# Kernel tuning notes

Measured on AMD Instinct MI355X. Metric: run time of the kernel, lower is better.

Reference implementation:

```python
import jax, jax.numpy as jnp
import numpy as np
from jax.scipy.linalg import solve_triangular

B, T, HID = 1, 2048, 2048
HK, DK = 16, 96
HV, DV = 16, 192
KDIM, VDIM = HK * DK, HV * DV
KCONV = 4
CHUNK = 64
EPS = 1e-6


def setup_inputs():
    key = jax.random.key(0)
    ks = jax.random.split(key, 16)
    s = 0.02
    return {
        "hidden_states": jax.random.normal(ks[0], (B, T, HID), jnp.float32),
        "Wq": jax.random.normal(ks[1], (HID, KDIM), jnp.float32) * s,
        "Wk": jax.random.normal(ks[2], (HID, KDIM), jnp.float32) * s,
        "Wv": jax.random.normal(ks[3], (HID, VDIM), jnp.float32) * s,
        "Wb": jax.random.normal(ks[4], (HID, HV), jnp.float32) * s,
        "Wa": jax.random.normal(ks[5], (HID, HV), jnp.float32) * s,
        "Wg": jax.random.normal(ks[6], (HID, VDIM), jnp.float32) * s,
        "Wo": jax.random.normal(ks[7], (VDIM, HID), jnp.float32) * s,
        "conv_q": jax.random.normal(ks[8], (KDIM, KCONV), jnp.float32) * 0.5,
        "conv_k": jax.random.normal(ks[9], (KDIM, KCONV), jnp.float32) * 0.5,
        "conv_v": jax.random.normal(ks[10], (VDIM, KCONV), jnp.float32) * 0.5,
        "A_log": jnp.log(jax.random.uniform(ks[11], (HV,), jnp.float32, 1.0, 16.0)),
        "dt_bias": jax.random.uniform(ks[12], (HV,), jnp.float32, 0.0, 1.0),
        "norm_weight": jnp.ones((DV,), jnp.float32),
    }


def short_conv_silu(x, w):
    # x: [B,T,C], w: [C,K]; causal depthwise conv (left pad K-1) then SiLU
    K = w.shape[-1]
    xp = jnp.pad(x, ((0, 0), (K - 1, 0), (0, 0)))
    y = sum(xp[:, j:j + x.shape[1], :] * w[:, j] for j in range(K))
    return jax.nn.silu(y)


def l2norm(x):
    return x * jax.lax.rsqrt(jnp.sum(x * x, axis=-1, keepdims=True) + EPS)


def chunk_gated_delta_rule(q, k, v, g, beta):
    # q,k: [B,T,H,dk]; v: [B,T,H,dv]; g,beta: [B,T,H]. Chunked parallel scan (WY form).
    Bb, Tt, H, dk = q.shape
    dv = v.shape[-1]
    N = Tt // CHUNK
    q = l2norm(q) * (dk ** -0.5)
    k = l2norm(k)
    chunk = lambda x: x.transpose(0, 2, 1, 3).reshape(Bb, H, N, CHUNK, x.shape[-1])
    qc, kc, vc = chunk(q), chunk(k), chunk(v)
    gc = jnp.cumsum(g.transpose(0, 2, 1).reshape(Bb, H, N, CHUNK), axis=-1)
    bc = beta.transpose(0, 2, 1).reshape(Bb, H, N, CHUNK)

    m_inc = jnp.tril(jnp.ones((CHUNK, CHUNK), bool))
    m_str = jnp.tril(jnp.ones((CHUNK, CHUNK), bool), -1)
    diff = gc[..., :, None] - gc[..., None, :]
    D = jnp.exp(jnp.where(m_inc, diff, 0.0)) * m_inc  # [B,H,N,C,C] intra-chunk decay

    kb = kc * bc[..., None]
    A = -jnp.einsum('bhnik,bhnjk->bhnij', kb, kc) * D * m_str
    eye = jnp.eye(CHUNK, dtype=q.dtype)
    # UT transform: Tm = (I - A)^{-1}, A strictly lower triangular
    Tm = solve_triangular(eye - A, jnp.broadcast_to(eye, A.shape), lower=True, unit_diagonal=True)
    u = Tm @ (vc * bc[..., None])                   # [B,H,N,C,dv]
    w = Tm @ (kb * jnp.exp(gc)[..., None])          # [B,H,N,C,dk]
    g_last = gc[..., -1]                            # [B,H,N]

    def step(S, inp):
        q_i, k_i, u_i, w_i, g_i, D_i, gl = inp
        v_new = u_i - w_i @ S                       # [B,H,C,dv]
        attn = jnp.einsum('bhik,bhjk->bhij', q_i, k_i) * D_i
        o_i = (q_i * jnp.exp(g_i)[..., None]) @ S + attn @ v_new
        k_dec = k_i * jnp.exp(gl[..., None] - g_i)[..., None]
        S = S * jnp.exp(gl)[..., None, None] + jnp.einsum('bhck,bhcv->bhkv', k_dec, v_new)
        return S, o_i

    mv = lambda x: jnp.moveaxis(x, 2, 0)
    S0 = jnp.zeros((Bb, H, dk, dv), q.dtype)
    _, o = jax.lax.scan(step, S0, (mv(qc), mv(kc), mv(u), mv(w), mv(gc), mv(D), mv(g_last)))
    o = jnp.moveaxis(o, 0, 2).reshape(Bb, H, Tt, dv)
    return o.transpose(0, 2, 1, 3)                  # [B,T,H,dv]


def reference(hidden_states, Wq, Wk, Wv, Wb, Wa, Wg, Wo, conv_q, conv_k, conv_v, A_log, dt_bias, norm_weight):
    q = short_conv_silu(hidden_states @ Wq, conv_q).reshape(B, T, HK, DK)
    k = short_conv_silu(hidden_states @ Wk, conv_k).reshape(B, T, HK, DK)
    v = short_conv_silu(hidden_states @ Wv, conv_v).reshape(B, T, HV, DV)
    beta = jax.nn.sigmoid(hidden_states @ Wb) * 2.0          # allow_neg_eigval -> beta in [0,2]
    g = -jnp.exp(A_log) * jax.nn.softplus(hidden_states @ Wa + dt_bias)  # log decay, [B,T,HV]
    o = chunk_gated_delta_rule(q, k, v, g, beta)             # [B,T,HV,DV]
    gate = (hidden_states @ Wg).reshape(B, T, HV, DV)
    o = o * jax.nn.silu(gate)                                # gated RMSNorm (gate, then norm)
    o = o * jax.lax.rsqrt(jnp.mean(o * o, axis=-1, keepdims=True) + EPS) * norm_weight
    return o.reshape(B, T, VDIM) @ Wo
```

## Files before the change

### kernel.cpp

```cpp
#include <hip/hip_runtime.h>
#include <math.h>

#define T_LEN 2048
#define HIDN  2048
#define HKN   16
#define DKN   96
#define HVN   16
#define DVN   192
#define KDIMN 1536
#define VDIMN 3072
#define QKVD  6144
#define CHUNKN 64
#define NCHUNK 32
#define EPSF 1e-6f
#define TN_STRIDE 10240

typedef __attribute__((ext_vector_type(8))) short short8;
typedef __attribute__((ext_vector_type(4))) float f32x4;

__device__ __forceinline__ unsigned short f2bf(float f) {
    unsigned int u = __float_as_uint(f);
    unsigned int r = (u + 0x7FFFu + ((u >> 16) & 1u)) >> 16;
    return (unsigned short)r;
}
__device__ __forceinline__ float bf2f(unsigned short u) {
    return __uint_as_float(((unsigned int)u) << 16);
}
__device__ __forceinline__ float siluf(float x) { return x / (1.f + expf(-x)); }

__device__ __forceinline__ void gld_lds16(const void* g, void* l) {
    __builtin_amdgcn_global_load_lds((const __attribute__((address_space(1))) unsigned int*)g,
                                     (__attribute__((address_space(3))) unsigned int*)l, 16, 0, 0);
}

__global__ void cast_f32_bf16(const float* __restrict__ in, unsigned short* __restrict__ out, int n) {
    int i = (blockIdx.x * blockDim.x + threadIdx.x) * 4;
    if (i >= n) return;
    float4 v = *(const float4*)(in + i);
    ushort4 o;
    o.x = f2bf(v.x); o.y = f2bf(v.y); o.z = f2bf(v.z); o.w = f2bf(v.w);
    *(ushort4*)(out + i) = o;
}

__global__ void transpose_cast(const float* __restrict__ W, unsigned short* __restrict__ Wt,
                               int K, int N) {
    __shared__ float tile[64][65];
    int k0 = blockIdx.y * 64, n0 = blockIdx.x * 64;
    int tx = threadIdx.x, ty = threadIdx.y;
    for (int r = ty; r < 64; r += 4) tile[r][tx] = W[(size_t)(k0 + r) * N + n0 + tx];
    __syncthreads();
    for (int r = ty; r < 64; r += 4) Wt[(size_t)(n0 + r) * K + k0 + tx] = f2bf(tile[tx][r]);
}

__global__ __launch_bounds__(256) void gemm_bt2(const unsigned short* __restrict__ A,
                                                const unsigned short* __restrict__ Bt,
                                                float* __restrict__ C1, int ld1, int nblk1,
                                                unsigned short* __restrict__ C2, int ld2,
                                                int M, int K) {
    __shared__ __align__(16) unsigned short As[2][128 * 32];
    __shared__ __align__(16) unsigned short Bs[2][128 * 32];
    int tid = threadIdx.x;
    int wave = tid >> 6, lane = tid & 63;
    int bm = blockIdx.y, bn = blockIdx.x;
    f32x4 acc[4][4] = {};
    int wr = wave >> 1, wc = wave & 1;
    int rstage = wave * 32 + (lane >> 2);
    int cstage = (lane & 3) * 8;
    const size_t a_row0 = (size_t)bm * 128;
    const size_t b_row0 = (size_t)bn * 128;
    const unsigned short* gaBase = A + (a_row0 + rstage) * (size_t)K + cstage;
    const unsigned short* gbBase = Bt + (b_row0 + rstage) * (size_t)K + cstage;
    int row_a[4], row_b[4];
#pragma unroll
    for (int i = 0; i < 4; ++i) {
        row_a[i] = wr * 64 + i * 16 + (lane & 15);
        row_b[i] = wc * 64 + i * 16 + (lane & 15);
    }
    int koff = (lane >> 4) * 8;
    int niter = K >> 5;
    {
        unsigned short* ab = &As[0][wave * 1024];
        unsigned short* bb = &Bs[0][wave * 1024];
        gld_lds16(gaBase, ab);
        gld_lds16(gaBase + (size_t)16 * K, ab + 512);
        gld_lds16(gbBase, bb);
        gld_lds16(gbBase + (size_t)16 * K, bb + 512);
    }
    __syncthreads();
    for (int i = 0; i < niter; ++i) {
        int cur = i & 1;
        if (i + 1 < niter) {
            int k0 = (i + 1) * 32;
            unsigned short* ab = &As[cur ^ 1][wave * 1024];
            unsigned short* bb = &Bs[cur ^ 1][wave * 1024];
            gld_lds16(gaBase + k0, ab);
            gld_lds16(gaBase + k0 + (size_t)16 * K, ab + 512);
            gld_lds16(gbBase + k0, bb);
            gld_lds16(gbBase + k0 + (size_t)16 * K, bb + 512);
        }
        short8 af[4], bfr[4];
#pragma unroll
        for (int mi = 0; mi < 4; ++mi) af[mi] = *(const short8*)&As[cur][row_a[mi] * 32 + koff];
#pragma unroll
        for (int ni = 0; ni < 4; ++ni) bfr[ni] = *(const short8*)&Bs[cur][row_b[ni] * 32 + koff];
#pragma unroll
        for (int mi = 0; mi < 4; ++mi)
#pragma unroll
            for (int ni = 0; ni < 4; ++ni)
                acc[mi][ni] = __builtin_amdgcn_mfma_f32_16x16x32_bf16(af[mi], bfr[ni], acc[mi][ni], 0, 0, 0);
        __syncthreads();
    }
    if (bn < nblk1) {
        int colb = bn * 128;
#pragma unroll
        for (int mi = 0; mi < 4; ++mi) {
            int rbase = bm * 128 + wr * 64 + mi * 16 + (lane >> 4) * 4;
#pragma unroll
            for (int ni = 0; ni < 4; ++ni) {
                int col = colb + wc * 64 + ni * 16 + (lane & 15);
#pragma unroll
                for (int j = 0; j < 4; ++j)
                    C1[(size_t)(rbase + j) * ld1 + col] = acc[mi][ni][j];
            }
        }
    } else {
        int colb = (bn - nblk1) * 128;
#pragma unroll
        for (int mi = 0; mi < 4; ++mi) {
            int rbase = bm * 128 + wr * 64 + mi * 16 + (lane >> 4) * 4;
#pragma unroll
            for (int ni = 0; ni < 4; ++ni) {
                int col = colb + wc * 64 + ni * 16 + (lane & 15);
#pragma unroll
                for (int j = 0; j < 4; ++j)
                    C2[(size_t)(rbase + j) * ld2 + col] = f2bf(acc[mi][ni][j]);
            }
        }
    }
}

__global__ __launch_bounds__(256) void gemm_btk(const unsigned short* __restrict__ A,
                                                const unsigned short* __restrict__ Bt,
                                                float* __restrict__ C, float* __restrict__ Cp,
                                                int M, int N, int K) {
    __shared__ __align__(16) unsigned short As[2][128 * 32];
    __shared__ __align__(16) unsigned short Bs[2][128 * 32];
    int tid = threadIdx.x;
    int wave = tid >> 6, lane = tid & 63;
    int bm = blockIdx.y, bn = blockIdx.x, kz = blockIdx.z;
    int kchunk = K / 3;
    int kbeg = kz * kchunk;
    f32x4 acc[4][4] = {};
    int wr = wave >> 1, wc = wave & 1;
    int rstage = wave * 32 + (lane >> 2);
    int cstage = (lane & 3) * 8;
    const size_t a_row0 = (size_t)bm * 128;
    const size_t b_row0 = (size_t)bn * 128;
    const unsigned short* gaBase = A + (a_row0 + rstage) * (size_t)K + kbeg + cstage;
    const unsigned short* gbBase = Bt + (b_row0 + rstage) * (size_t)K + kbeg + cstage;
    int row_a[4], row_b[4];
#pragma unroll
    for (int i = 0; i < 4; ++i) {
        row_a[i] = wr * 64 + i * 16 + (lane & 15);
        row_b[i] = wc * 64 + i * 16 + (lane & 15);
    }
    int koff = (lane >> 4) * 8;
    int niter = kchunk >> 5;
    {
        unsigned short* ab = &As[0][wave * 1024];
        unsigned short* bb = &Bs[0][wave * 1024];
        gld_lds16(gaBase, ab);
        gld_lds16(gaBase + (size_t)16 * K, ab + 512);
        gld_lds16(gbBase, bb);
        gld_lds16(gbBase + (size_t)16 * K, bb + 512);
    }
    __syncthreads();
    for (int i = 0; i < niter; ++i) {
        int cur = i & 1;
        if (i + 1 < niter) {
            int k0 = (i + 1) * 32;
            unsigned short* ab = &As[cur ^ 1][wave * 1024];
            unsigned short* bb = &Bs[cur ^ 1][wave * 1024];
            gld_lds16(gaBase + k0, ab);
            gld_lds16(gaBase + k0 + (size_t)16 * K, ab + 512);
            gld_lds16(gbBase + k0, bb);
            gld_lds16(gbBase + k0 + (size_t)16 * K, bb + 512);
        }
        short8 af[4], bfr[4];
#pragma unroll
        for (int mi = 0; mi < 4; ++mi) af[mi] = *(const short8*)&As[cur][row_a[mi] * 32 + koff];
#pragma unroll
        for (int ni = 0; ni < 4; ++ni) bfr[ni] = *(const short8*)&Bs[cur][row_b[ni] * 32 + koff];
#pragma unroll
        for (int mi = 0; mi < 4; ++mi)
#pragma unroll
            for (int ni = 0; ni < 4; ++ni)
                acc[mi][ni] = __builtin_amdgcn_mfma_f32_16x16x32_bf16(af[mi], bfr[ni], acc[mi][ni], 0, 0, 0);
        __syncthreads();
    }
    float* Cout = (kz == 0) ? C : (Cp + (size_t)(kz - 1) * M * N);
#pragma unroll
    for (int mi = 0; mi < 4; ++mi) {
        int rbase = bm * 128 + wr * 64 + mi * 16 + (lane >> 4) * 4;
#pragma unroll
        for (int ni = 0; ni < 4; ++ni) {
            int col = bn * 128 + wc * 64 + ni * 16 + (lane & 15);
#pragma unroll
            for (int j = 0; j < 4; ++j)
                Cout[(size_t)(rbase + j) * N + col] = acc[mi][ni][j];
        }
    }
}

__global__ void addk(float* __restrict__ out, const float* __restrict__ p, int n) {
    int i = (blockIdx.x * blockDim.x + threadIdx.x) * 4;
    if (i >= n) return;
    float4 a = *(const float4*)(out + i);
    float4 b = *(const float4*)(p + i);
    float4 c = *(const float4*)(p + n + i);
    a.x += b.x + c.x; a.y += b.y + c.y; a.z += b.z + c.z; a.w += b.w + c.w;
    *(float4*)(out + i) = a;
}

__global__ void conv_silu_all(const float* __restrict__ pre,
                              const float* __restrict__ cq, const float* __restrict__ ck,
                              const float* __restrict__ cv, float* __restrict__ out) {
    int c = blockIdx.x * blockDim.x + threadIdx.x;
    int t = blockIdx.y;
    const float* wc4 = (c < 1536) ? (cq + (size_t)c * 4)
                     : (c < 3072) ? (ck + (size_t)(c - 1536) * 4)
                                  : (cv + (size_t)(c - 3072) * 4);
    float acc = 0.f;
    if (t >= 3) acc += pre[(size_t)(t - 3) * QKVD + c] * wc4[0];
    if (t >= 2) acc += pre[(size_t)(t - 2) * QKVD + c] * wc4[1];
    if (t >= 1) acc += pre[(size_t)(t - 1) * QKVD + c] * wc4[2];
    acc += pre[(size_t)t * QKVD + c] * wc4[3];
    out[(size_t)t * QKVD + c] = siluf(acc);
}

__global__ __launch_bounds__(256) void beta_g(const float* __restrict__ X,
                                              const float* __restrict__ Wb, const float* __restrict__ Wa,
                                              const float* __restrict__ A_log, const float* __restrict__ dtb,
                                              float* __restrict__ bvec, float* __restrict__ gvec) {
    int t = blockIdx.x;
    int tid = threadIdx.x;
    int cg = tid & 7, ks = tid >> 3;
    int wave = tid >> 6, lane = tid & 63;
    const float* xr = X + (size_t)t * HIDN;
    const float* Wsel = (cg < 4) ? Wb : Wa;
    int cc = (cg & 3) * 4;
    float ax = 0.f, ay = 0.f, az = 0.f, aw = 0.f;
#pragma unroll 4
    for (int i = 0; i < 16; ++i) {
        int k = (ks + 32 * i) * 4;
        float4 xv = *(const float4*)(xr + k);
        float4 w0 = *(const float4*)(Wsel + (size_t)(k + 0) * 16 + cc);
        float4 w1 = *(const float4*)(Wsel + (size_t)(k + 1) * 16 + cc);
        float4 w2 = *(const float4*)(Wsel + (size_t)(k + 2) * 16 + cc);
        float4 w3 = *(const float4*)(Wsel + (size_t)(k + 3) * 16 + cc);
        ax += xv.x * w0.x + xv.y * w1.x + xv.z * w2.x + xv.w * w3.x;
        ay += xv.x * w0.y + xv.y * w1.y + xv.z * w2.y + xv.w * w3.y;
        az += xv.x * w0.z + xv.y * w1.z + xv.z * w2.z + xv.w * w3.z;
        aw += xv.x * w0.w + xv.y * w1.w + xv.z * w2.w + xv.w * w3.w;
    }
#pragma unroll
    for (int off = 8; off <= 32; off <<= 1) {
        ax += __shfl_xor(ax, off, 64);
        ay += __shfl_xor(ay, off, 64);
        az += __shfl_xor(az, off, 64);
        aw += __shfl_xor(aw, off, 64);
    }
    __shared__ float red[4][8][4];
    if ((lane >> 3) == 0) {
        red[wave][cg][0] = ax; red[wave][cg][1] = ay;
        red[wave][cg][2] = az; red[wave][cg][3] = aw;
    }
    __syncthreads();
    if (tid < 8) {
        float tot[4];
#pragma unroll
        for (int j = 0; j < 4; ++j)
            tot[j] = red[0][tid][j] + red[1][tid][j] + red[2][tid][j] + red[3][tid][j];
        int c0 = (tid & 3) * 4;
        if (tid < 4) {
#pragma unroll
            for (int j = 0; j < 4; ++j)
                bvec[(size_t)t * 16 + c0 + j] = 2.f / (1.f + expf(-tot[j]));
        } else {
#pragma unroll
            for (int j = 0; j < 4; ++j) {
                float a = tot[j] + dtb[c0 + j];
                float sp = (a > 20.f) ? a : log1pf(expf(a));
                gvec[(size_t)t * 16 + c0 + j] = -expf(A_log[c0 + j]) * sp;
            }
        }
    }
}

__global__ __launch_bounds__(256) void phase1_mfma(
    const float* __restrict__ qkv, const float* __restrict__ gvec,
    const float* __restrict__ bvec,
    float* __restrict__ u_ws, float* __restrict__ w_ws,
    float* __restrict__ qg_ws, float* __restrict__ at_ws,
    float* __restrict__ gl_ws, float* __restrict__ Ct,
    unsigned short* __restrict__ Tn) {
    int n = blockIdx.x, h = blockIdx.y;
    int t0 = n * CHUNKN;
    int tid = threadIdx.x;
    int wave = tid >> 6, lane = tid & 63;
    size_t base = (size_t)(h * NCHUNK + n);

    __shared__ __align__(16) char LB1[139776];
    unsigned short* QKb  = (unsigned short*)(LB1 + 0);
    unsigned short* Pb   = (unsigned short*)(LB1 + 26624);
    unsigned short* RHSw = (unsigned short*)(LB1 + 39936);
    unsigned short* RHSv = (unsigned short*)(LB1 + 53760);
    unsigned short* Ab   = (unsigned short*)(LB1 + 81408);
    unsigned short* Atb  = (unsigned short*)(LB1 + 94720);
    unsigned short* Ptb  = (unsigned short*)(LB1 + 108032);
    float*          Pf   = (float*)(LB1 + 121344);
    unsigned short* kdT  = (unsigned short*)(LB1 + 81408);
    unsigned short* wT   = (unsigned short*)(LB1 + 95232);
    unsigned short* uT   = (unsigned short*)(LB1 + 109056);
    float* gr_s = (float*)(LB1 + 138752);
    float* gc_s = gr_s + 64;
    float* be_s = gc_s + 64;
    float* egc  = be_s + 64;

    if (tid < 64) {
        gr_s[tid] = gvec[(size_t)(t0 + tid) * HVN + h];
        be_s[tid] = bvec[(size_t)(t0 + tid) * HVN + h];
    }
    __syncthreads();
    if (tid < 64) {
        float sacc = 0.f;
        for (int j = 0; j <= tid; ++j) sacc += gr_s[j];
        gc_s[tid] = sacc;
    }
    __syncthreads();
    float gl = gc_s[63];
    if (tid < 64) egc[tid] = expf(gl - gc_s[tid]);

    int r = tid >> 2, sub = tid & 3;
    {
        const float* kp = qkv + (size_t)(t0 + r) * QKVD + 1536 + h * DKN + sub * 24;
        float kreg[24];
        float ss = 0.f;
#pragma unroll
        for (int i = 0; i < 6; ++i) {
            float4 v = *(const float4*)(kp + i * 4);
            kreg[i * 4 + 0] = v.x; kreg[i * 4 + 1] = v.y; kreg[i * 4 + 2] = v.z; kreg[i * 4 + 3] = v.w;
            ss += v.x * v.x + v.y * v.y + v.z * v.z + v.w * v.w;
        }
        ss += __shfl_xor(ss, 1, 64);
        ss += __shfl_xor(ss, 2, 64);
        float nrm = rsqrtf(ss + EPSF);
        float gcr = gc_s[r];
        float ebg = be_s[r] * expf(gcr);
#pragma unroll
        for (int i = 0; i < 24; ++i) {
            float kn = kreg[i] * nrm;
            QKb[r * 104 + sub * 24 + i] = f2bf(kn);
            RHSw[(sub * 24 + i) * 72 + r] = f2bf(kn * ebg);
        }
    }
    {
        const float* qp = qkv + (size_t)(t0 + r) * QKVD + 0 + h * DKN + sub * 24;
        float qreg[24];
        float ss = 0.f;
#pragma unroll
        for (int i = 0; i < 6; ++i) {
            float4 v = *(const float4*)(qp + i * 4);
            qreg[i * 4 + 0] = v.x; qreg[i * 4 + 1] = v.y; qreg[i * 4 + 2] = v.z; qreg[i * 4 + 3] = v.w;
            ss += v.x * v.x + v.y * v.y + v.z * v.z + v.w * v.w;
        }
        ss += __shfl_xor(ss, 1, 64);
        ss += __shfl_xor(ss, 2, 64);
        float nrm = rsqrtf(ss + EPSF) * 0.10206207261596577f;
        float eg = expf(gc_s[r]);
        float* qgp = qg_ws + base * (64 * 96) + r * 96 + sub * 24;
#pragma unroll
        for (int i = 0; i < 24; ++i) {
            float qn = qreg[i] * nrm;
            QKb[(64 + r) * 104 + sub * 24 + i] = f2bf(qn);
            qgp[i] = qn * eg;
        }
    }
    {
        const float* vp = qkv + (size_t)(t0 + r) * QKVD + 3072 + h * DVN + sub * 48;
        float ber = be_s[r];
#pragma unroll
        for (int i = 0; i < 12; ++i) {
            float4 v = *(const float4*)(vp + i * 4);
            int d = sub * 48 + i * 4;
            RHSv[(d + 0) * 72 + r] = f2bf(v.x * ber);
            RHSv[(d + 1) * 72 + r] = f2bf(v.y * ber);
            RHSv[(d + 2) * 72 + r] = f2bf(v.z * ber);
            RHSv[(d + 3) * 72 + r] = f2bf(v.w * ber);
        }
    }
    __syncthreads();

    {
        f32x4 acc1[2][4] = {};
#pragma unroll
        for (int ks = 0; ks < 3; ++ks) {
            int ko = ks * 32 + (lane >> 4) * 8;
            short8 af[2], bfv[4];
#pragma unroll
            for (int rt2 = 0; rt2 < 2; ++rt2)
                af[rt2] = *(const short8*)&QKb[(wave * 32 + rt2 * 16 + (lane & 15)) * 104 + ko];
#pragma unroll
            for (int ct = 0; ct < 4; ++ct)
                bfv[ct] = *(const short8*)&QKb[(ct * 16 + (lane & 15)) * 104 + ko];
#pragma unroll
            for (int rt2 = 0; rt2 < 2; ++rt2)
#pragma unroll
                for (int ct = 0; ct < 4; ++ct)
                    acc1[rt2][ct] = __builtin_amdgcn_mfma_f32_16x16x32_bf16(af[rt2], bfv[ct], acc1[rt2][ct], 0, 0, 0);
        }
#pragma unroll
        for (int rt2 = 0; rt2 < 2; ++rt2)
#pragma unroll
            for (int ct = 0; ct < 4; ++ct)
#pragma unroll
                for (int j = 0; j < 4; ++j) {
                    int rr = wave * 32 + rt2 * 16 + (lane >> 4) * 4 + j;
                    int cc = ct * 16 + (lane & 15);
                    float val = acc1[rt2][ct][j];
                    if (rr < 64) {
                        float av = (rr > cc) ? -be_s[rr] * expf(gc_s[rr] - gc_s[cc]) * val : 0.f;
                        unsigned short ab = f2bf(av);
                        Ab[rr * 104 + cc] = ab;
                        Atb[cc * 104 + rr] = ab;
                        float pv = (rr == cc) ? 1.f : av;
                        Pf[rr * 68 + cc] = pv;
                        unsigned short pb = f2bf(pv);
                        Pb[rr * 104 + cc] = pb;
                        Ptb[cc * 104 + rr] = pb;
                    } else {
                        int ar = rr - 64;
                        float av = (ar >= cc) ? expf(gc_s[ar] - gc_s[cc]) * val : 0.f;
                        at_ws[base * (64 * 64) + ar * 64 + cc] = av;
                    }
                }
    }
    __syncthreads();

#pragma unroll 1
    for (int lev = 0; lev < 5; ++lev) {
        f32x4 d[4] = {};
#pragma unroll
        for (int ks = 0; ks < 2; ++ks) {
            int ko = ks * 32 + (lane >> 4) * 8;
            short8 a0 = *(const short8*)&Ab[(wave * 16 + (lane & 15)) * 104 + ko];
#pragma unroll
            for (int ct = 0; ct < 4; ++ct) {
                short8 b0 = *(const short8*)&Atb[(ct * 16 + (lane & 15)) * 104 + ko];
                d[ct] = __builtin_amdgcn_mfma_f32_16x16x32_bf16(a0, b0, d[ct], 0, 0, 0);
            }
        }
        __syncthreads();
#pragma unroll
        for (int ct = 0; ct < 4; ++ct)
#pragma unroll
            for (int j = 0; j < 4; ++j) {
                int rr = wave * 16 + (lane >> 4) * 4 + j;
                int cc = ct * 16 + (lane & 15);
                unsigned short hb = f2bf(d[ct][j]);
                Ab[rr * 104 + cc] = hb;
                Atb[cc * 104 + rr] = hb;
            }
        __syncthreads();
        f32x4 e[4];
#pragma unroll
        for (int ct = 0; ct < 4; ++ct)
#pragma unroll
            for (int j = 0; j < 4; ++j)
                e[ct][j] = Pf[(wave * 16 + (lane >> 4) * 4 + j) * 68 + ct * 16 + (lane & 15)];
#pragma unroll
        for (int ks = 0; ks < 2; ++ks) {
            int ko = ks * 32 + (lane >> 4) * 8;
            short8 a0 = *(const short8*)&Ab[(wave * 16 + (lane & 15)) * 104 + ko];
#pragma unroll
            for (int ct = 0; ct < 4; ++ct) {
                short8 b0 = *(const short8*)&Ptb[(ct * 16 + (lane & 15)) * 104 + ko];
                e[ct] = __builtin_amdgcn_mfma_f32_16x16x32_bf16(a0, b0, e[ct], 0, 0, 0);
            }
        }
        __syncthreads();
#pragma unroll
        for (int ct = 0; ct < 4; ++ct)
#pragma unroll
            for (int j = 0; j < 4; ++j) {
                int rr = wave * 16 + (lane >> 4) * 4 + j;
                int cc = ct * 16 + (lane & 15);
                float pv = e[ct][j];
                Pf[rr * 68 + cc] = pv;
                unsigned short pb = f2bf(pv);
                Pb[rr * 104 + cc] = pb;
                Ptb[cc * 104 + rr] = pb;
            }
        __syncthreads();
    }

    for (int f = tid; f < 6144; f += 256) {
        int d = f >> 6, tt = f & 63;
        kdT[d * 72 + tt] = f2bf(bf2f(QKb[tt * 104 + d]) * egc[tt]);
    }

#pragma unroll 1
    for (int i = 0; i < 18; ++i) {
        int id = wave * 18 + i;
        int rt = id & 3, ct = id >> 2;
        f32x4 o4 = {};
#pragma unroll
        for (int ks = 0; ks < 2; ++ks) {
            int ko = ks * 32 + (lane >> 4) * 8;
            short8 a0 = *(const short8*)&Pb[(rt * 16 + (lane & 15)) * 104 + ko];
            short8 b0 = (ct < 12)
                ? *(const short8*)&RHSv[(ct * 16 + (lane & 15)) * 72 + ko]
                : *(const short8*)&RHSw[((ct - 12) * 16 + (lane & 15)) * 72 + ko];
            o4 = __builtin_amdgcn_mfma_f32_16x16x32_bf16(a0, b0, o4, 0, 0, 0);
        }
#pragma unroll
        for (int j = 0; j < 4; ++j) {
            int rr = rt * 16 + (lane >> 4) * 4 + j;
            int nn = ct * 16 + (lane & 15);
            if (ct < 12) {
                u_ws[base * (64 * 192) + rr * 192 + nn] = o4[j];
                uT[nn * 72 + rr] = f2bf(o4[j]);
            } else {
                w_ws[base * (64 * 96) + rr * 96 + (nn - 192)] = o4[j];
                wT[(nn - 192) * 72 + rr] = f2bf(o4[j]);
            }
        }
    }
    __syncthreads();

    float eglv = expf(gl);
#pragma unroll 1
    for (int q = 0; q < 27; ++q) {
        int id = wave * 27 + q;
        f32x4 acc = {};
        if (id < 36) {
            int jt = id / 6, kt = id % 6;
#pragma unroll
            for (int ks = 0; ks < 2; ++ks) {
                int ko = ks * 32 + (lane >> 4) * 8;
                short8 a0 = *(const short8*)&kdT[(jt * 16 + (lane & 15)) * 72 + ko];
                short8 b0 = *(const short8*)&wT[(kt * 16 + (lane & 15)) * 72 + ko];
                acc = __builtin_amdgcn_mfma_f32_16x16x32_bf16(a0, b0, acc, 0, 0, 0);
            }
#pragma unroll
            for (int rr = 0; rr < 4; ++rr) {
                int j = jt * 16 + (lane >> 4) * 4 + rr;
                int k = kt * 16 + (lane & 15);
                float val = -acc[rr];
                if (j == k) val += eglv;
                Tn[base * TN_STRIDE + j * 104 + k] = f2bf(val);
            }
        } else {
            int cid = id - 36;
            int it = cid / 6, jt = cid % 6;
#pragma unroll
            for (int ks = 0; ks < 2; ++ks) {
                int ko = ks * 32 + (lane >> 4) * 8;
                short8 a0 = *(const short8*)&uT[(it * 16 + (lane & 15)) * 72 + ko];
                short8 b0 = *(const short8*)&kdT[(jt * 16 + (lane & 15)) * 72 + ko];
                acc = __builtin_amdgcn_mfma_f32_16x16x32_bf16(a0, b0, acc, 0, 0, 0);
            }
#pragma unroll
            for (int rr = 0; rr < 4; ++rr)
                Ct[base * 18432 + (size_t)(it * 16 + (lane >> 4) * 4 + rr) * 96 + jt * 16 + (lane & 15)] = acc[rr];
        }
    }
    if (tid == 0) gl_ws[base] = gl;
}

__global__ __launch_bounds__(128) void mscan(const float* __restrict__ Ct, const unsigned short* __restrict__ Tn,
                                             float* __restrict__ s_ws) {
    int rg = blockIdx.x, h = blockIdx.y;
    int tid = threadIdx.x, wave = tid >> 6, lane = tid & 63;
    __shared__ __align__(16) unsigned short St[48 * 104];
    __shared__ __align__(16) unsigned short TnB[2][TN_STRIDE];
    __shared__ __align__(16) float CtB[2][48 * 96];
    for (int i = tid; i < 48 * 104; i += 128) St[i] = 0;

    {
        const float* cp = Ct + (size_t)(h * NCHUNK) * 18432 + rg * (48 * 96);
        const unsigned short* tp = Tn + (size_t)(h * NCHUNK) * TN_STRIDE;
#pragma unroll
        for (int q = 0; q < 9; ++q) {
            size_t o = (size_t)(wave * 9 + q) * 1024 + lane * 16;
            gld_lds16((const char*)cp + o, (char*)&CtB[0][0] + (size_t)(wave * 9 + q) * 1024);
        }
#pragma unroll
        for (int q = 0; q < 10; ++q) {
            size_t o = (size_t)(wave * 10 + q) * 1024 + lane * 16;
            gld_lds16((const char*)tp + o, (char*)&TnB[0][0] + (size_t)(wave * 10 + q) * 1024);
        }
    }
    f32x4 acc[3][3] = {};
    int colw = wave * 48;
    __syncthreads();

#pragma unroll 1
    for (int n = 0; n < NCHUNK; ++n) {
        size_t base = (size_t)(h * NCHUNK + n);
        int cur = n & 1;
        if (n + 1 < NCHUNK) {
            const float* cp = Ct + (base + 1) * 18432 + rg * (48 * 96);
            const unsigned short* tp = Tn + (base + 1) * TN_STRIDE;
#pragma unroll
            for (int q = 0; q < 9; ++q) {
                size_t o = (size_t)(wave * 9 + q) * 1024 + lane * 16;
                gld_lds16((const char*)cp + o, (char*)&CtB[cur ^ 1][0] + (size_t)(wave * 9 + q) * 1024);
            }
#pragma unroll
            for (int q = 0; q < 10; ++q) {
                size_t o = (size_t)(wave * 10 + q) * 1024 + lane * 16;
                gld_lds16((const char*)tp + o, (char*)&TnB[cur ^ 1][0] + (size_t)(wave * 10 + q) * 1024);
            }
        }
        float* sp = s_ws + base * 18432 + rg * (48 * 96);
#pragma unroll
        for (int it = 0; it < 3; ++it)
#pragma unroll
            for (int jt = 0; jt < 3; ++jt) {
                int irow = it * 16 + (lane >> 4) * 4;
                int col = colw + jt * 16 + (lane & 15);
#pragma unroll
                for (int r = 0; r < 4; ++r) {
                    sp[(size_t)(irow + r) * 96 + col] = acc[it][jt][r];
                    acc[it][jt][r] = CtB[cur][(irow + r) * 96 + col];
                }
            }
#pragma unroll
        for (int ks = 0; ks < 3; ++ks) {
            int ko = ks * 32 + (lane >> 4) * 8;
            short8 af[3], bfv[3];
#pragma unroll
            for (int it = 0; it < 3; ++it)
                af[it] = *(const short8*)&St[(it * 16 + (lane & 15)) * 104 + ko];
#pragma unroll
            for (int jt = 0; jt < 3; ++jt)
                bfv[jt] = *(const short8*)&TnB[cur][(colw + jt * 16 + (lane & 15)) * 104 + ko];
#pragma unroll
            for (int it = 0; it < 3; ++it)
#pragma unroll
                for (int jt = 0; jt < 3; ++jt)
                    acc[it][jt] = __builtin_amdgcn_mfma_f32_16x16x32_bf16(af[it], bfv[jt], acc[it][jt], 0, 0, 0);
        }
        __syncthreads();
#pragma unroll
        for (int it = 0; it < 3; ++it)
#pragma unroll
            for (int jt = 0; jt < 3; ++jt)
#pragma unroll
                for (int r = 0; r < 4; ++r)
                    St[(it * 16 + (lane >> 4) * 4 + r) * 104 + colw + jt * 16 + (lane & 15)] = f2bf(acc[it][jt][r]);
        __syncthreads();
    }
}

#define P2_ST 0
#define P2_W  39936
#define P2_QG 53248
#define P2_AT 66560
#define P2_U  75776
#define P2_VN 125952
__global__ __launch_bounds__(256) void phase2b_mfma(const float* __restrict__ s_ws, const float* __restrict__ w_ws,
                                                    const float* __restrict__ qg_ws, const float* __restrict__ at_ws,
                                                    const float* __restrict__ u_ws,
                                                    const unsigned short* __restrict__ Cgate,
                                                    const float* __restrict__ nw,
                                                    unsigned short* __restrict__ obf) {
    __shared__ __align__(16) char LB[153600];
    unsigned short* StB = (unsigned short*)(LB + P2_ST);
    unsigned short* wB  = (unsigned short*)(LB + P2_W);
    unsigned short* qgB = (unsigned short*)(LB + P2_QG);
    unsigned short* atB = (unsigned short*)(LB + P2_AT);
    float* uF           = (float*)(LB + P2_U);
    unsigned short* vnB = (unsigned short*)(LB + P2_VN);
    int n = blockIdx.x, h = blockIdx.y;
    size_t base = (size_t)(h * NCHUNK + n);
    int tid = threadIdx.x, wave = tid >> 6, lane = tid & 63;
    int i0w = wave * 48;
    {
        const float* sp = s_ws + base * 18432;
        for (int f = tid; f < 4608; f += 256) {
            int i = f / 24, c4 = (f % 24) * 4;
            float4 v = *(const float4*)(sp + i * 96 + c4);
            ushort4 o4; o4.x = f2bf(v.x); o4.y = f2bf(v.y); o4.z = f2bf(v.z); o4.w = f2bf(v.w);
            *(ushort4*)&StB[i * 104 + c4] = o4;
        }
    }
    {
        const float* wp = w_ws + base * 6144;
        const float* qp = qg_ws + base * 6144;
        for (int f = tid; f < 1536; f += 256) {
            int t = f / 24, c4 = (f % 24) * 4;
            float4 wv = *(const float4*)(wp + t * 96 + c4);
            float4 qv = *(const float4*)(qp + t * 96 + c4);
            ushort4 ow; ow.x = f2bf(-wv.x); ow.y = f2bf(-wv.y); ow.z = f2bf(-wv.z); ow.w = f2bf(-wv.w);
            ushort4 oq; oq.x = f2bf(qv.x); oq.y = f2bf(qv.y); oq.z = f2bf(qv.z); oq.w = f2bf(qv.w);
            *(ushort4*)&wB[t * 104 + c4] = ow;
            *(ushort4*)&qgB[t * 104 + c4] = oq;
        }
    }
    {
        const float* ap = at_ws + base * 4096;
        for (int f = tid; f < 1024; f += 256) {
            int t = f / 16, c4 = (f % 16) * 4;
            float4 av = *(const float4*)(ap + t * 64 + c4);
            ushort4 oa; oa.x = f2bf(av.x); oa.y = f2bf(av.y); oa.z = f2bf(av.z); oa.w = f2bf(av.w);
            *(ushort4*)&atB[t * 72 + c4] = oa;
        }
    }
    {
        const float* up = u_ws + base * 12288;
        for (int f = tid; f < 3072; f += 256) {
            int t = f / 48, c4 = (f % 48) * 4;
            *(float4*)&uF[t * 196 + c4] = *(const float4*)(up + t * 192 + c4);
        }
    }
    __syncthreads();
    {
        f32x4 acc[3][4];
#pragma unroll
        for (int it = 0; it < 3; ++it)
#pragma unroll
            for (int jt = 0; jt < 4; ++jt)
#pragma unroll
                for (int r = 0; r < 4; ++r)
                    acc[it][jt][r] = uF[(jt * 16 + (lane & 15)) * 196 + i0w + it * 16 + (lane >> 4) * 4 + r];
#pragma unroll
        for (int ks = 0; ks < 3; ++ks) {
            int ko = ks * 32 + (lane >> 4) * 8;
            short8 af[3], bfv[4];
#pragma unroll
            for (int it = 0; it < 3; ++it)
                af[it] = *(const short8*)&StB[(i0w + it * 16 + (lane & 15)) * 104 + ko];
#pragma unroll
            for (int jt = 0; jt < 4; ++jt)
                bfv[jt] = *(const short8*)&wB[(jt * 16 + (lane & 15)) * 104 + ko];
#pragma unroll
            for (int it = 0; it < 3; ++it)
#pragma unroll
                for (int jt = 0; jt < 4; ++jt)
                    acc[it][jt] = __builtin_amdgcn_mfma_f32_16x16x32_bf16(af[it], bfv[jt], acc[it][jt], 0, 0, 0);
        }
#pragma unroll
        for (int it = 0; it < 3; ++it)
#pragma unroll
            for (int jt = 0; jt < 4; ++jt)
#pragma unroll
                for (int r = 0; r < 4; ++r)
                    vnB[(i0w + it * 16 + (lane >> 4) * 4 + r) * 72 + jt * 16 + (lane & 15)] = f2bf(acc[it][jt][r]);
    }
    f32x4 acc2[3][4] = {};
#pragma unroll
    for (int ks = 0; ks < 3; ++ks) {
        int ko = ks * 32 + (lane >> 4) * 8;
        short8 af[3], bfv[4];
#pragma unroll
        for (int it = 0; it < 3; ++it)
            af[it] = *(const short8*)&StB[(i0w + it * 16 + (lane & 15)) * 104 + ko];
#pragma unroll
        for (int jt = 0; jt < 4; ++jt)
            bfv[jt] = *(const short8*)&qgB[(jt * 16 + (lane & 15)) * 104 + ko];
#pragma unroll
        for (int it = 0; it < 3; ++it)
#pragma unroll
            for (int jt = 0; jt < 4; ++jt)
                acc2[it][jt] = __builtin_amdgcn_mfma_f32_16x16x32_bf16(af[it], bfv[jt], acc2[it][jt], 0, 0, 0);
    }
#pragma unroll
    for (int ks = 0; ks < 2; ++ks) {
        int ko = ks * 32 + (lane >> 4) * 8;
        short8 af[3], bfv[4];
#pragma unroll
        for (int it = 0; it < 3; ++it)
            af[it] = *(const short8*)&vnB[(i0w + it * 16 + (lane & 15)) * 72 + ko];
#pragma unroll
        for (int jt = 0; jt < 4; ++jt)
            bfv[jt] = *(const short8*)&atB[(jt * 16 + (lane & 15)) * 72 + ko];
#pragma unroll
        for (int it = 0; it < 3; ++it)
#pragma unroll
            for (int jt = 0; jt < 4; ++jt)
                acc2[it][jt] = __builtin_amdgcn_mfma_f32_16x16x32_bf16(af[it], bfv[jt], acc2[it][jt], 0, 0, 0);
    }
    __syncthreads();
    float* oF = (float*)(LB + 0);
#pragma unroll
    for (int it = 0; it < 3; ++it)
#pragma unroll
        for (int jt = 0; jt < 4; ++jt)
#pragma unroll
            for (int r = 0; r < 4; ++r)
                oF[(i0w + it * 16 + (lane >> 4) * 4 + r) * 68 + jt * 16 + (lane & 15)] = acc2[it][jt][r];
    __syncthreads();

    float* ssq = (float*)(LB + 131072);
    float* rno = (float*)(LB + 132096);
    int jj = tid >> 2, qq = tid & 3;
    int t0 = n * CHUNKN;
    {
        const unsigned short* gp = Cgate + (size_t)(t0 + jj) * VDIMN + h * DVN + qq * 48;
        float ss = 0.f;
#pragma unroll 4
        for (int m = 0; m < 48; ++m) {
            int i = qq * 48 + m;
            float x = oF[i * 68 + jj];
            float g = bf2f(gp[m]);
            float xv = x * siluf(g);
            oF[i * 68 + jj] = xv;
            ss += xv * xv;
        }
        ssq[jj * 4 + qq] = ss;
    }
    __syncthreads();
    if (tid < 64) {
        float tot = ssq[tid * 4] + ssq[tid * 4 + 1] + ssq[tid * 4 + 2] + ssq[tid * 4 + 3];
        rno[tid] = rsqrtf(tot * (1.f / 192.f) + EPSF);
    }
    __syncthreads();
    {
        float rr2 = rno[jj];
        unsigned short* op = obf + (size_t)(t0 + jj) * VDIMN + h * DVN + qq * 48;
#pragma unroll 4
        for (int m = 0; m < 48; ++m) {
            int i = qq * 48 + m;
            op[m] = f2bf(oF[i * 68 + jj] * rr2 * nw[i]);
        }
    }
}

extern "C" void kernel_launch(void* const* d_in, const int* in_sizes, int n_in,
                              void* d_out, int out_size, void* d_ws, size_t ws_size,
                              hipStream_t stream) {
    (void)in_sizes; (void)n_in; (void)out_size;
    const float* X    = (const float*)d_in[0];
    const float* Wq   = (const float*)d_in[1];
    const float* Wk   = (const float*)d_in[2];
    const float* Wv   = (const float*)d_in[3];
    const float* Wb   = (const float*)d_in[4];
    const float* Wa   = (const float*)d_in[5];
    const float* Wg   = (const float*)d_in[6];
    const float* Wo   = (const float*)d_in[7];
    const float* cq   = (const float*)d_in[8];
    const float* ck   = (const float*)d_in[9];
    const float* cv   = (const float*)d_in[10];
    const float* Alog = (const float*)d_in[11];
    const float* dtb  = (const float*)d_in[12];
    const float* nw   = (const float*)d_in[13];

    const size_t OFF_XBF   = 0;
    const size_t OFF_WALLT = 8388608;
    const size_t OFF_WOT   = 46137344;
    const size_t OFF_CQKV  = 58720256;
    const size_t OFF_CGATE = 109051904;
    const size_t OFF_QPOST = 134217728;
    const size_t OFF_GVEC  = 184549376;
    const size_t OFF_BVEC  = 184680448;
    const size_t OFF_GL    = 184811520;
    const size_t OFF_U     = 184819712;
    const size_t OFF_W     = 209985536;
    const size_t OFF_QG    = 222568448;
    const size_t OFF_KD    = 235151360;
    const size_t OFF_AT    = OFF_XBF;
    const size_t OFF_CT    = OFF_CQKV;
    const size_t OFF_TN    = OFF_CQKV + 37748736;
    const size_t OFF_S     = OFF_QPOST;
    const size_t OFF_OBF   = OFF_WALLT + 25165824;
    const size_t OFF_OPART = OFF_CQKV;
    const size_t NEEDED    = 247734272;
    if (ws_size < NEEDED) return;

    char* ws = (char*)d_ws;
    unsigned short* Xbf   = (unsigned short*)(ws + OFF_XBF);
    unsigned short* WallT = (unsigned short*)(ws + OFF_WALLT);
    unsigned short* WoT   = (unsigned short*)(ws + OFF_WOT);
    float* Cqkv  = (float*)(ws + OFF_CQKV);
    unsigned short* Cgate = (unsigned short*)(ws + OFF_CGATE);
    float* qkvpost = (float*)(ws + OFF_QPOST);
    float* gvec  = (float*)(ws + OFF_GVEC);
    float* bvec  = (float*)(ws + OFF_BVEC);
    float* gl_ws = (float*)(ws + OFF_GL);
    float* u_ws  = (float*)(ws + OFF_U);
    float* w_ws  = (float*)(ws + OFF_W);
    float* qg_ws = (float*)(ws + OFF_QG);
    float* at_ws = (float*)(ws + OFF_AT);
    float* Ct    = (float*)(ws + OFF_CT);
    unsigned short* Tn = (unsigned short*)(ws + OFF_TN);
    float* s_ws  = (float*)(ws + OFF_S);
    unsigned short* obf = (unsigned short*)(ws + OFF_OBF);
    float* opart = (float*)(ws + OFF_OPART);

    cast_f32_bf16<<<4096, 256, 0, stream>>>(X, Xbf, 2048 * 2048);
    dim3 tb(64, 4);
    transpose_cast<<<dim3(1536 / 64, 2048 / 64), tb, 0, stream>>>(Wq, WallT, 2048, 1536);
    transpose_cast<<<dim3(1536 / 64, 2048 / 64), tb, 0, stream>>>(Wk, WallT + (size_t)1536 * 2048, 2048, 1536);
    transpose_cast<<<dim3(3072 / 64, 2048 / 64), tb, 0, stream>>>(Wv, WallT + (size_t)3072 * 2048, 2048, 3072);
    transpose_cast<<<dim3(3072 / 64, 2048 / 64), tb, 0, stream>>>(Wg, WallT + (size_t)6144 * 2048, 2048, 3072);
    transpose_cast<<<dim3(2048 / 64, 3072 / 64), tb, 0, stream>>>(Wo, WoT, 3072, 2048);

    gemm_bt2<<<dim3(9216 / 128, 2048 / 128), 256, 0, stream>>>(Xbf, WallT,
                                                               Cqkv, QKVD, QKVD / 128,
                                                               Cgate, VDIMN, 2048, 2048);

    conv_silu_all<<<dim3(QKVD / 256, T_LEN), 256, 0, stream>>>(Cqkv, cq, ck, cv, qkvpost);
    beta_g<<<T_LEN, 256, 0, stream>>>(X, Wb, Wa, Alog, dtb, bvec, gvec);

    phase1_mfma<<<dim3(NCHUNK, HVN), 256, 0, stream>>>(qkvpost, gvec, bvec,
                                                       u_ws, w_ws, qg_ws, at_ws, gl_ws, Ct, Tn);
    mscan<<<dim3(4, HVN), 128, 0, stream>>>(Ct, Tn, s_ws);
    phase2b_mfma<<<dim3(NCHUNK, HVN), 256, 0, stream>>>(s_ws, w_ws, qg_ws, at_ws, u_ws,
                                                        Cgate, nw, obf);

    gemm_btk<<<dim3(2048 / 128, 2048 / 128, 3), 256, 0, stream>>>(obf, WoT, (float*)d_out, opart,
                                                                  2048, 2048, 3072);
    addk<<<4096, 256, 0, stream>>>((float*)d_out, opart, 2048 * 2048);
}
```

Measured before the change: 463.9 us.

## Fuse causal conv+SiLU into phase1 and merge weight transpose launches

Removes the standalone conv_silu kernel and its full-size intermediate buffer. phase1 now computes the 4-tap causal conv and SiLU on the fly from the raw projection output, with per-head conv weights staged in shared memory. The five transpose-cast launches are merged into one kernel that picks its source by block index. Workspace offsets are rearranged so Ct and Tn no longer alias Cqkv, which phase1 now reads. The cost is redundant reloads of neighbouring rows and more shared memory in phase1.

Result: faster. 413.5 us (-10.9%).

```diff
diff --git a/kernel.cpp b/kernel.cpp
--- a/kernel.cpp
+++ b/kernel.cpp
@@ -42,10 +42,20 @@
     *(ushort4*)(out + i) = o;
 }
 
-__global__ void transpose_cast(const float* __restrict__ W, unsigned short* __restrict__ Wt,
-                               int K, int N) {
+__global__ void prep_weights(const float* __restrict__ Wq, const float* __restrict__ Wk,
+                             const float* __restrict__ Wv, const float* __restrict__ Wg,
+                             const float* __restrict__ Wo,
+                             unsigned short* __restrict__ WallT, unsigned short* __restrict__ WoT) {
     __shared__ float tile[64][65];
-    int k0 = blockIdx.y * 64, n0 = blockIdx.x * 64;
+    int bid = blockIdx.x;
+    const float* W; unsigned short* Wt; int K, N, l;
+    if (bid < 768)       { W = Wq; Wt = WallT;                          K = 2048; N = 1536; l = bid; }
+    else if (bid < 1536) { W = Wk; Wt = WallT + (size_t)1536 * 2048;    K = 2048; N = 1536; l = bid - 768; }
+    else if (bid < 3072) { W = Wv; Wt = WallT + (size_t)3072 * 2048;    K = 2048; N = 3072; l = bid - 1536; }
+    else if (bid < 4608) { W = Wg; Wt = WallT + (size_t)6144 * 2048;    K = 2048; N = 3072; l = bid - 3072; }
+    else                 { W = Wo; Wt = WoT;                            K = 3072; N = 2048; l = bid - 4608; }
+    int nbx = N >> 6;
+    int n0 = (l % nbx) * 64, k0 = (l / nbx) * 64;
     int tx = threadIdx.x, ty = threadIdx.y;
     for (int r = ty; r < 64; r += 4) tile[r][tx] = W[(size_t)(k0 + r) * N + n0 + tx];
     __syncthreads();
@@ -220,22 +230,6 @@
     float4 c = *(const float4*)(p + n + i);
     a.x += b.x + c.x; a.y += b.y + c.y; a.z += b.z + c.z; a.w += b.w + c.w;
     *(float4*)(out + i) = a;
-}
-
-__global__ void conv_silu_all(const float* __restrict__ pre,
-                              const float* __restrict__ cq, const float* __restrict__ ck,
-                              const float* __restrict__ cv, float* __restrict__ out) {
-    int c = blockIdx.x * blockDim.x + threadIdx.x;
-    int t = blockIdx.y;
-    const float* wc4 = (c < 1536) ? (cq + (size_t)c * 4)
-                     : (c < 3072) ? (ck + (size_t)(c - 1536) * 4)
-                                  : (cv + (size_t)(c - 3072) * 4);
-    float acc = 0.f;
-    if (t >= 3) acc += pre[(size_t)(t - 3) * QKVD + c] * wc4[0];
-    if (t >= 2) acc += pre[(size_t)(t - 2) * QKVD + c] * wc4[1];
-    if (t >= 1) acc += pre[(size_t)(t - 1) * QKVD + c] * wc4[2];
-    acc += pre[(size_t)t * QKVD + c] * wc4[3];
-    out[(size_t)t * QKVD + c] = siluf(acc);
 }
 
 __global__ __launch_bounds__(256) void beta_g(const float* __restrict__ X,
@@ -298,8 +292,9 @@
 }
 
 __global__ __launch_bounds__(256) void phase1_mfma(
-    const float* __restrict__ qkv, const float* __restrict__ gvec,
-    const float* __restrict__ bvec,
+    const float* __restrict__ Cqkv,
+    const float* __restrict__ cq, const float* __restrict__ ck, const float* __restrict__ cv,
+    const float* __restrict__ gvec, const float* __restrict__ bvec,
     float* __restrict__ u_ws, float* __restrict__ w_ws,
     float* __restrict__ qg_ws, float* __restrict__ at_ws,
     float* __restrict__ gl_ws, float* __restrict__ Ct,
@@ -326,7 +321,14 @@
     float* gc_s = gr_s + 64;
     float* be_s = gc_s + 64;
     float* egc  = be_s + 64;
-
+    __shared__ __align__(16) float cwS[384 * 4];
+
+    for (int f = tid; f < 384; f += 256) {
+        const float* src = (f < 96)  ? (cq + (size_t)(h * 96 + f) * 4)
+                         : (f < 192) ? (ck + (size_t)(h * 96 + f - 96) * 4)
+                                     : (cv + (size_t)(h * 192 + f - 192) * 4);
+        *(float4*)&cwS[f * 4] = *(const float4*)src;
+    }
     if (tid < 64) {
         gr_s[tid] = gvec[(size_t)(t0 + tid) * HVN + h];
         be_s[tid] = bvec[(size_t)(t0 + tid) * HVN + h];
@@ -342,21 +344,32 @@
     if (tid < 64) egc[tid] = expf(gl - gc_s[tid]);
 
     int r = tid >> 2, sub = tid & 3;
-    {
-        const float* kp = qkv + (size_t)(t0 + r) * QKVD + 1536 + h * DKN + sub * 24;
+    int trow = t0 + r;
+    {
+        int gc0 = 1536 + h * DKN + sub * 24;
+        int lc0 = 96 + sub * 24;
         float kreg[24];
         float ss = 0.f;
 #pragma unroll
         for (int i = 0; i < 6; ++i) {
-            float4 v = *(const float4*)(kp + i * 4);
-            kreg[i * 4 + 0] = v.x; kreg[i * 4 + 1] = v.y; kreg[i * 4 + 2] = v.z; kreg[i * 4 + 3] = v.w;
-            ss += v.x * v.x + v.y * v.y + v.z * v.z + v.w * v.w;
+            float4 x0 = (trow >= 3) ? *(const float4*)(Cqkv + (size_t)(trow - 3) * QKVD + gc0 + i * 4) : make_float4(0, 0, 0, 0);
+            float4 x1 = (trow >= 2) ? *(const float4*)(Cqkv + (size_t)(trow - 2) * QKVD + gc0 + i * 4) : make_float4(0, 0, 0, 0);
+            float4 x2 = (trow >= 1) ? *(const float4*)(Cqkv + (size_t)(trow - 1) * QKVD + gc0 + i * 4) : make_float4(0, 0, 0, 0);
+            float4 x3 = *(const float4*)(Cqkv + (size_t)trow * QKVD + gc0 + i * 4);
+#pragma unroll
+            for (int c = 0; c < 4; ++c) {
+                float4 w = *(const float4*)&cwS[(lc0 + i * 4 + c) * 4];
+                float xv = ((const float*)&x0)[c] * w.x + ((const float*)&x1)[c] * w.y
+                         + ((const float*)&x2)[c] * w.z + ((const float*)&x3)[c] * w.w;
+                xv = siluf(xv);
+                kreg[i * 4 + c] = xv;
+                ss += xv * xv;
+            }
         }
         ss += __shfl_xor(ss, 1, 64);
         ss += __shfl_xor(ss, 2, 64);
         float nrm = rsqrtf(ss + EPSF);
-        float gcr = gc_s[r];
-        float ebg = be_s[r] * expf(gcr);
+        float ebg = be_s[r] * expf(gc_s[r]);
 #pragma unroll
         for (int i = 0; i < 24; ++i) {
             float kn = kreg[i] * nrm;
@@ -365,14 +378,25 @@
         }
     }
     {
-        const float* qp = qkv + (size_t)(t0 + r) * QKVD + 0 + h * DKN + sub * 24;
+        int gc0 = h * DKN + sub * 24;
+        int lc0 = sub * 24;
         float qreg[24];
         float ss = 0.f;
 #pragma unroll
         for (int i = 0; i < 6; ++i) {
-            float4 v = *(const float4*)(qp + i * 4);
-            qreg[i * 4 + 0] = v.x; qreg[i * 4 + 1] = v.y; qreg[i * 4 + 2] = v.z; qreg[i * 4 + 3] = v.w;
-            ss += v.x * v.x + v.y * v.y + v.z * v.z + v.w * v.w;
+            float4 x0 = (trow >= 3) ? *(const float4*)(Cqkv + (size_t)(trow - 3) * QKVD + gc0 + i * 4) : make_float4(0, 0, 0, 0);
+            float4 x1 = (trow >= 2) ? *(const float4*)(Cqkv + (size_t)(trow - 2) * QKVD + gc0 + i * 4) : make_float4(0, 0, 0, 0);
+            float4 x2 = (trow >= 1) ? *(const float4*)(Cqkv + (size_t)(trow - 1) * QKVD + gc0 + i * 4) : make_float4(0, 0, 0, 0);
+            float4 x3 = *(const float4*)(Cqkv + (size_t)trow * QKVD + gc0 + i * 4);
+#pragma unroll
+            for (int c = 0; c < 4; ++c) {
+                float4 w = *(const float4*)&cwS[(lc0 + i * 4 + c) * 4];
+                float xv = ((const float*)&x0)[c] * w.x + ((const float*)&x1)[c] * w.y
+                         + ((const float*)&x2)[c] * w.z + ((const float*)&x3)[c] * w.w;
+                xv = siluf(xv);
+                qreg[i * 4 + c] = xv;
+                ss += xv * xv;
+            }
         }
         ss += __shfl_xor(ss, 1, 64);
         ss += __shfl_xor(ss, 2, 64);
@@ -387,16 +411,22 @@
         }
     }
     {
-        const float* vp = qkv + (size_t)(t0 + r) * QKVD + 3072 + h * DVN + sub * 48;
+        int gc0 = 3072 + h * DVN + sub * 48;
+        int lc0 = 192 + sub * 48;
         float ber = be_s[r];
 #pragma unroll
         for (int i = 0; i < 12; ++i) {
-            float4 v = *(const float4*)(vp + i * 4);
-            int d = sub * 48 + i * 4;
-            RHSv[(d + 0) * 72 + r] = f2bf(v.x * ber);
-            RHSv[(d + 1) * 72 + r] = f2bf(v.y * ber);
-            RHSv[(d + 2) * 72 + r] = f2bf(v.z * ber);
-            RHSv[(d + 3) * 72 + r] = f2bf(v.w * ber);
+            float4 x0 = (trow >= 3) ? *(const float4*)(Cqkv + (size_t)(trow - 3) * QKVD + gc0 + i * 4) : make_float4(0, 0, 0, 0);
+            float4 x1 = (trow >= 2) ? *(const float4*)(Cqkv + (size_t)(trow - 2) * QKVD + gc0 + i * 4) : make_float4(0, 0, 0, 0);
+            float4 x2 = (trow >= 1) ? *(const float4*)(Cqkv + (size_t)(trow - 1) * QKVD + gc0 + i * 4) : make_float4(0, 0, 0, 0);
+            float4 x3 = *(const float4*)(Cqkv + (size_t)trow * QKVD + gc0 + i * 4);
+#pragma unroll
+            for (int c = 0; c < 4; ++c) {
+                float4 w = *(const float4*)&cwS[(lc0 + i * 4 + c) * 4];
+                float xv = ((const float*)&x0)[c] * w.x + ((const float*)&x1)[c] * w.y
+                         + ((const float*)&x2)[c] * w.z + ((const float*)&x3)[c] * w.w;
+                RHSv[(sub * 48 + i * 4 + c) * 72 + r] = f2bf(siluf(xv) * ber);
+            }
         }
     }
     __syncthreads();
@@ -862,21 +892,19 @@
     const size_t OFF_WOT   = 46137344;
     const size_t OFF_CQKV  = 58720256;
     const size_t OFF_CGATE = 109051904;
-    const size_t OFF_QPOST = 134217728;
+    const size_t OFF_CT    = 134217728;
+    const size_t OFF_TN    = OFF_CT + 37748736;
     const size_t OFF_GVEC  = 184549376;
     const size_t OFF_BVEC  = 184680448;
     const size_t OFF_GL    = 184811520;
     const size_t OFF_U     = 184819712;
     const size_t OFF_W     = 209985536;
     const size_t OFF_QG    = 222568448;
-    const size_t OFF_KD    = 235151360;
     const size_t OFF_AT    = OFF_XBF;
-    const size_t OFF_CT    = OFF_CQKV;
-    const size_t OFF_TN    = OFF_CQKV + 37748736;
-    const size_t OFF_S     = OFF_QPOST;
+    const size_t OFF_S     = OFF_CQKV;
     const size_t OFF_OBF   = OFF_WALLT + 25165824;
     const size_t OFF_OPART = OFF_CQKV;
-    const size_t NEEDED    = 247734272;
+    const size_t NEEDED    = 235151360;
     if (ws_size < NEEDED) return;
 
     char* ws = (char*)d_ws;
@@ -885,7 +913,6 @@
     unsigned short* WoT   = (unsigned short*)(ws + OFF_WOT);
     float* Cqkv  = (float*)(ws + OFF_CQKV);
     unsigned short* Cgate = (unsigned short*)(ws + OFF_CGATE);
-    float* qkvpost = (float*)(ws + OFF_QPOST);
     float* gvec  = (float*)(ws + OFF_GVEC);
     float* bvec  = (float*)(ws + OFF_BVEC);
     float* gl_ws = (float*)(ws + OFF_GL);
@@ -900,21 +927,15 @@
     float* opart = (float*)(ws + OFF_OPART);
 
     cast_f32_bf16<<<4096, 256, 0, stream>>>(X, Xbf, 2048 * 2048);
-    dim3 tb(64, 4);
-    transpose_cast<<<dim3(1536 / 64, 2048 / 64), tb, 0, stream>>>(Wq, WallT, 2048, 1536);
-    transpose_cast<<<dim3(1536 / 64, 2048 / 64), tb, 0, stream>>>(Wk, WallT + (size_t)1536 * 2048, 2048, 1536);
-    transpose_cast<<<dim3(3072 / 64, 2048 / 64), tb, 0, stream>>>(Wv, WallT + (size_t)3072 * 2048, 2048, 3072);
-    transpose_cast<<<dim3(3072 / 64, 2048 / 64), tb, 0, stream>>>(Wg, WallT + (size_t)6144 * 2048, 2048, 3072);
-    transpose_cast<<<dim3(2048 / 64, 3072 / 64), tb, 0, stream>>>(Wo, WoT, 3072, 2048);
+    prep_weights<<<6144, dim3(64, 4), 0, stream>>>(Wq, Wk, Wv, Wg, Wo, WallT, WoT);
 
     gemm_bt2<<<dim3(9216 / 128, 2048 / 128), 256, 0, stream>>>(Xbf, WallT,
                                                                Cqkv, QKVD, QKVD / 128,
                                                                Cgate, VDIMN, 2048, 2048);
 
-    conv_silu_all<<<dim3(QKVD / 256, T_LEN), 256, 0, stream>>>(Cqkv, cq, ck, cv, qkvpost);
     beta_g<<<T_LEN, 256, 0, stream>>>(X, Wb, Wa, Alog, dtb, bvec, gvec);
 
-    phase1_mfma<<<dim3(NCHUNK, HVN), 256, 0, stream>>>(qkvpost, gvec, bvec,
+    phase1_mfma<<<dim3(NCHUNK, HVN), 256, 0, stream>>>(Cqkv, cq, ck, cv, gvec, bvec,
                                                        u_ws, w_ws, qg_ws, at_ws, gl_ws, Ct, Tn);
     mscan<<<dim3(4, HVN), 128, 0, stream>>>(Ct, Tn, s_ws);
     phase2b_mfma<<<dim3(NCHUNK, HVN), 256, 0, stream>>>(s_ws, w_ws, qg_ws, at_ws, u_ws,
```
